# Performance work log

Measured on AMD Instinct MI355X. Metric: run time of the kernel, lower is better.

The kernel has to match this reference:

```python
import jax, jax.numpy as jnp
import numpy as np

B, G, IN, F, O = 65536, 6, 512, 256, 18


def setup_inputs() -> dict:
    key = jax.random.key(0)
    ks = jax.random.split(key, 9)
    return {
        "state": jax.random.normal(ks[0], (B, IN), dtype=jnp.float32),
        "action": jax.random.randint(ks[1], (B, 1), 0, O, dtype=jnp.int64),
        "idx": jax.random.randint(ks[2], (B,), 0, G, dtype=jnp.int64),
        # per-game expert Linear weights (stored [in, out] so fwd is x @ W)
        "W1": jax.random.normal(ks[3], (G, IN, F), dtype=jnp.float32) * (1.0 / np.sqrt(IN)),
        "b1": jnp.zeros((G, F), dtype=jnp.float32),
        # shared layer
        "W2": jax.random.normal(ks[4], (F, F), dtype=jnp.float32) * (1.0 / np.sqrt(F)),
        "b2": jnp.zeros((F,), dtype=jnp.float32),
        # per-game Q heads
        "Wq": jax.random.normal(ks[5], (G, F, O), dtype=jnp.float32) * (1.0 / np.sqrt(F)),
        "bq": jnp.zeros((G, O), dtype=jnp.float32),
    }


def reference(state, action, idx, W1, b1, W2, b2, Wq, bq):
    # The torch code processes samples grouped by np.unique(idx) and then
    # torch.cat's the groups: this is a stable sort of samples by idx value.
    perm = jnp.argsort(idx)  # jnp.argsort is stable by default
    sp = state[perm]         # [B, IN], samples in group-sorted order
    ip = idx[perm]           # [B]

    # per-game expert: compute all G tiny linears, select the routed one
    h_all = jax.nn.sigmoid(jnp.einsum('bi,gif->bgf', sp, W1) + b1)  # [B,G,F]
    h1 = jnp.take_along_axis(h_all, ip[:, None, None], axis=1)[:, 0, :]  # [B,F]

    # shared layer ('relu' branch)
    h_f = jax.nn.relu(h1 @ W2 + b2)  # [B,F]

    # stacked per-game heads
    q = jnp.tanh(jnp.einsum('bf,gfo->bgo', h_f, Wq) + bq)  # [B,G,O]

    # action gather: q_acted[b,g] = q[b,g,action[b,0]] (action in ORIGINAL order,
    # exactly as in the torch code, which gathers on the permuted-row q)
    a = jnp.broadcast_to(action[:, :1], (B, G))[..., None]  # [B,G,1]
    q_acted = jnp.take_along_axis(q, a, axis=2)[..., 0]     # [B,G]

    # idx gather (again with idx in ORIGINAL order, matching the torch code)
    q_out = jnp.take_along_axis(q_acted, idx[:, None], axis=1)[:, 0]  # [B]
    return q_out
```

## Files before the change

kernel.cpp:

```cpp
#include <hip/hip_runtime.h>
#include <math.h>

#define B_N 65536
#define G_N 6
#define IN_N 512
#define F_N 256
#define O_N 18

#define NB 256
#define CHUNK 256

#define TBM 64
#define MAXT 1030

typedef __bf16 bf16x8 __attribute__((ext_vector_type(8)));
typedef float f32x4 __attribute__((ext_vector_type(4)));

#define WS_BC     0
#define WS_BOFF   8192
#define WS_NTILES 16448
#define WS_DESC   16512
#define WS_W1F    65536
#define WS_W2F    (WS_W1F + 1572864)
#define WS_WQT    (WS_W2F + 131072)
#define WS_PERM   4194304

__device__ __forceinline__ unsigned short f2bf(float f) {
    union { float f; unsigned u; } a; a.f = f;
    unsigned r = a.u + 0x7fffu + ((a.u >> 16) & 1u);
    return (unsigned short)(r >> 16);
}
__device__ __forceinline__ unsigned pack2(float a, float b) {
    return (unsigned)f2bf(a) | ((unsigned)f2bf(b) << 16);
}
__device__ __forceinline__ bf16x8 asbf(uint4 u) {
    union { uint4 u; bf16x8 b; } c; c.u = u; return c.b;
}

__global__ void k_hist(const int* __restrict__ idx, int* __restrict__ bc) {
    __shared__ int cnt[G_N];
    int t = threadIdx.x;
    if (t < G_N) cnt[t] = 0;
    __syncthreads();
    int e = blockIdx.x * CHUNK + t;
    atomicAdd(&cnt[idx[e]], 1);
    __syncthreads();
    if (t < G_N) bc[blockIdx.x * G_N + t] = cnt[t];
}

__global__ void k_prefix(const int* __restrict__ bc, int* __restrict__ boff,
                         int* __restrict__ ntiles, int* __restrict__ desc) {
    __shared__ int sbc[NB * G_N];
    __shared__ int tot[G_N], st[G_N];
    __shared__ int tstart[G_N + 1];
    int t = threadIdx.x;
    for (int i = t; i < NB * G_N; i += 256) sbc[i] = bc[i];
    __syncthreads();
    int w = t >> 6, l = t & 63;
    for (int g = w; g < G_N; g += 4) {
        int v[4]; int s = 0;
#pragma unroll
        for (int j = 0; j < 4; j++) { v[j] = sbc[(l * 4 + j) * G_N + g]; s += v[j]; }
        int inc = s;
#pragma unroll
        for (int o = 1; o < 64; o <<= 1) { int x = __shfl_up(inc, o, 64); if (l >= o) inc += x; }
        int run = inc - s;
        if (l == 63) tot[g] = inc;
#pragma unroll
        for (int j = 0; j < 4; j++) { sbc[(l * 4 + j) * G_N + g] = run; run += v[j]; }
    }
    __syncthreads();
    if (t == 0) {
        int acc = 0;
        for (int g = 0; g < G_N; g++) { st[g] = acc; acc += tot[g]; }
        int nt = 0;
        for (int g = 0; g < G_N; g++) { tstart[g] = nt; nt += (tot[g] + TBM - 1) / TBM; }
        tstart[G_N] = nt;
        *ntiles = nt;
    }
    __syncthreads();
    for (int i = t; i < NB * G_N; i += 256) boff[i] = sbc[i] + st[i % G_N];
    int nt = tstart[G_N];
    for (int i = t; i < MAXT; i += 256) {
        int gd = 0, r0 = 0, nr = 0;
        if (i < nt) {
            int g = 0;
            while (g < G_N - 1 && i >= tstart[g + 1]) g++;
            int k = i - tstart[g];
            r0 = st[g] + k * TBM;
            int rem = tot[g] - k * TBM;
            nr = rem < TBM ? rem : TBM;
            gd = g;
        }
        desc[i * 3 + 0] = gd; desc[i * 3 + 1] = r0; desc[i * 3 + 2] = nr;
    }
}

__global__ void k_scatter(const int* __restrict__ idx, const int* __restrict__ boff,
                          int* __restrict__ perm) {
    __shared__ int wcnt[4][G_N];
    __shared__ int base[G_N];
    int t = threadIdx.x, w = t >> 6, l = t & 63;
    int e = blockIdx.x * CHUNK + t;
    int g = idx[e];
    int rank = 0;
    for (int gg = 0; gg < G_N; gg++) {
        unsigned long long m = __ballot(g == gg);
        if (g == gg) rank = __popcll(m & ((1ull << l) - 1ull));
        if (l == 0) wcnt[w][gg] = __popcll(m);
    }
    if (t < G_N) base[t] = boff[blockIdx.x * G_N + t];
    __syncthreads();
    int off = base[g] + rank;
    for (int ww = 0; ww < w; ww++) off += wcnt[ww][g];
    perm[off] = e;
}

__global__ void k_pack(const float* __restrict__ src, unsigned short* __restrict__ dst,
                       long srcZ, long dstZ) {
    int kf = blockIdx.x, w = blockIdx.y, g = blockIdx.z;
    int kfTot = gridDim.x;
    int f = threadIdx.x >> 6, l = threadIdx.x & 63;
    int lrow = l & 15, q = l >> 4;
    int n = w * 32 + f * 16 + lrow;
    int k0 = kf * 32 + q * 8;
    const float* s = src + (long)g * srcZ + (long)k0 * F_N + n;
    unsigned o[4];
#pragma unroll
    for (int j = 0; j < 4; j++)
        o[j] = pack2(s[(2 * j) * F_N], s[(2 * j + 1) * F_N]);
    unsigned short* d = dst + (long)g * dstZ +
        ((((long)w * kfTot + kf) * 2 + f) * 64 + l) * 8;
    uint4 v = { o[0], o[1], o[2], o[3] };
    *(uint4*)d = v;
}

__global__ void k_wqt(const float* __restrict__ wq, float* __restrict__ wqt) {
    int g = blockIdx.x, f = threadIdx.x;
#pragma unroll
    for (int o = 0; o < O_N; o++)
        wqt[((long)g * O_N + o) * F_N + f] = wq[((long)g * F_N + f) * O_N + o];
}

__global__ __launch_bounds__(512, 4) void k_fused(
    const float* __restrict__ state, const char* __restrict__ w1f,
    const char* __restrict__ w2f, const float* __restrict__ wqt,
    const float* __restrict__ b1, const float* __restrict__ b2,
    const float* __restrict__ bqv,
    const int* __restrict__ action, const int* __restrict__ idx,
    const int* __restrict__ perm, const int* __restrict__ desc,
    float* __restrict__ out) {
    int td = blockIdx.x;
    int g = desc[td * 3 + 0], row0 = desc[td * 3 + 1], nr = desc[td * 3 + 2];
    if (nr == 0) return;

    __shared__ __align__(16) unsigned short smA[TBM * 512];
    __shared__ float partial[TBM][9];
    __shared__ int gq[TBM], actv[TBM];
    unsigned short* smH = smA;

    int t = threadIdx.x, w = t >> 6, l = t & 63;
    int lrow = l & 15, q = l >> 4;
    int x0 = lrow & 7;

    const char* B1 = w1f + (((long)g * 8 + w) << 15) + l * 16;
    uint4 nb0 = *(const uint4*)(B1);
    uint4 nb1 = *(const uint4*)(B1 + 1024);

    if (t < TBM) {
        int pos = row0 + t; if (pos > B_N - 1) pos = B_N - 1;
        gq[t] = idx[pos];
        actv[t] = action[pos];
    }

    {
        int m = t >> 3, s = t & 7;
        int pr = row0 + m; if (pr > B_N - 1) pr = B_N - 1;
        const float* src = state + (long)perm[pr] * IN_N + s * 4;
        int cb = s >> 1, h = s & 1, mx = m & 7;
        char* rowbase = (char*)smA + m * 1024 + h * 8;
#pragma unroll
        for (int j = 0; j < 16; j++) {
            float4 v = *(const float4*)(src + j * 32);
            uint2 p = { pack2(v.x, v.y), pack2(v.z, v.w) };
            int c = (cb + j * 4) ^ mx;
            *(uint2*)(rowbase + c * 16) = p;
        }
    }
    __syncthreads();

    const char* ar[4];
#pragma unroll
    for (int i = 0; i < 4; i++) ar[i] = (const char*)smA + (i * 16 + lrow) * 1024;

    f32x4 acc[4][2];
#pragma unroll
    for (int i = 0; i < 4; i++)
#pragma unroll
        for (int j = 0; j < 2; j++) acc[i][j] = (f32x4){0.f, 0.f, 0.f, 0.f};

#pragma unroll
    for (int kf = 0; kf < 16; kf++) {
        uint4 cb0 = nb0, cb1 = nb1;
        if (kf < 15) {
            nb0 = *(const uint4*)(B1 + (kf + 1) * 2048);
            nb1 = *(const uint4*)(B1 + (kf + 1) * 2048 + 1024);
        }
        int c = ((kf * 4 + q) ^ x0) * 16;
        bf16x8 af[4];
#pragma unroll
        for (int i = 0; i < 4; i++) af[i] = *(const bf16x8*)(ar[i] + c);
        bf16x8 b0 = asbf(cb0), b1v = asbf(cb1);
#pragma unroll
        for (int i = 0; i < 4; i++) {
            acc[i][0] = __builtin_amdgcn_mfma_f32_16x16x32_bf16(af[i], b0, acc[i][0], 0, 0, 0);
            acc[i][1] = __builtin_amdgcn_mfma_f32_16x16x32_bf16(af[i], b1v, acc[i][1], 0, 0, 0);
        }
    }
    __syncthreads();

    {
        int col0 = w * 32 + lrow;
#pragma unroll
        for (int j = 0; j < 2; j++) {
            int col = col0 + j * 16;
            float bias = b1[g * F_N + col];
            int cc = col >> 3, cb2 = (col & 7) * 2;
#pragma unroll
            for (int i = 0; i < 4; i++)
#pragma unroll
                for (int r = 0; r < 4; r++) {
                    int row = i * 16 + q * 4 + r;
                    float v = acc[i][j][r] + bias;
                    float sg = 1.0f / (1.0f + __expf(-v));
                    int c = cc ^ (row & 7);
                    *(unsigned short*)((char*)smH + row * 512 + c * 16 + cb2) = f2bf(sg);
                }
        }
    }
    __syncthreads();

    const char* B2 = w2f + ((long)w << 14) + l * 16;
    const char* hr[4];
#pragma unroll
    for (int i = 0; i < 4; i++) hr[i] = (const char*)smH + (i * 16 + lrow) * 512;

    f32x4 acc2[4][2];
#pragma unroll
    for (int i = 0; i < 4; i++)
#pragma unroll
        for (int j = 0; j < 2; j++) acc2[i][j] = (f32x4){0.f, 0.f, 0.f, 0.f};

    uint4 m0 = *(const uint4*)(B2);
    uint4 m1 = *(const uint4*)(B2 + 1024);
#pragma unroll
    for (int kf = 0; kf < 8; kf++) {
        uint4 c0 = m0, c1 = m1;
        if (kf < 7) {
            m0 = *(const uint4*)(B2 + (kf + 1) * 2048);
            m1 = *(const uint4*)(B2 + (kf + 1) * 2048 + 1024);
        }
        int c = ((kf * 4 + q) ^ x0) * 16;
        bf16x8 af[4];
#pragma unroll
        for (int i = 0; i < 4; i++) af[i] = *(const bf16x8*)(hr[i] + c);
        bf16x8 b0 = asbf(c0), b1v = asbf(c1);
#pragma unroll
        for (int i = 0; i < 4; i++) {
            acc2[i][0] = __builtin_amdgcn_mfma_f32_16x16x32_bf16(af[i], b0, acc2[i][0], 0, 0, 0);
            acc2[i][1] = __builtin_amdgcn_mfma_f32_16x16x32_bf16(af[i], b1v, acc2[i][1], 0, 0, 0);
        }
    }

    {
        int col0 = w * 32 + lrow;
        float bias0 = b2[col0], bias1 = b2[col0 + 16];
#pragma unroll
        for (int i = 0; i < 4; i++)
#pragma unroll
            for (int r = 0; r < 4; r++) {
                int row = i * 16 + q * 4 + r;
                const float* wp = wqt + ((long)gq[row] * O_N + actv[row]) * F_N;
                float v0 = fmaxf(acc2[i][0][r] + bias0, 0.0f);
                float v1 = fmaxf(acc2[i][1][r] + bias1, 0.0f);
                float s = v0 * wp[col0] + v1 * wp[col0 + 16];
                s += __shfl_xor(s, 1, 64);
                s += __shfl_xor(s, 2, 64);
                s += __shfl_xor(s, 4, 64);
                s += __shfl_xor(s, 8, 64);
                if (lrow == 0) partial[row][w] = s;
            }
    }
    __syncthreads();
    if (t < TBM && t < nr) {
        float s = 0.f;
#pragma unroll
        for (int ww = 0; ww < 8; ww++) s += partial[t][ww];
        out[row0 + t] = tanhf(s + bqv[gq[t] * O_N + actv[t]]);
    }
}

extern "C" void kernel_launch(void* const* d_in, const int* in_sizes, int n_in,
                              void* d_out, int out_size, void* d_ws, size_t ws_size,
                              hipStream_t stream) {
    const float* state  = (const float*)d_in[0];
    const int*   action = (const int*)d_in[1];
    const int*   idx    = (const int*)d_in[2];
    const float* W1     = (const float*)d_in[3];
    const float* b1     = (const float*)d_in[4];
    const float* W2     = (const float*)d_in[5];
    const float* b2     = (const float*)d_in[6];
    const float* Wq     = (const float*)d_in[7];
    const float* bq     = (const float*)d_in[8];
    float* out = (float*)d_out;

    char* ws = (char*)d_ws;
    int* bc      = (int*)(ws + WS_BC);
    int* boff    = (int*)(ws + WS_BOFF);
    int* ntiles  = (int*)(ws + WS_NTILES);
    int* desc    = (int*)(ws + WS_DESC);
    unsigned short* W1f = (unsigned short*)(ws + WS_W1F);
    unsigned short* W2f = (unsigned short*)(ws + WS_W2F);
    float* WqT   = (float*)(ws + WS_WQT);
    int* perm    = (int*)(ws + WS_PERM);

    k_hist<<<NB, CHUNK, 0, stream>>>(idx, bc);
    k_prefix<<<1, 256, 0, stream>>>(bc, boff, ntiles, desc);
    k_scatter<<<NB, CHUNK, 0, stream>>>(idx, boff, perm);
    k_pack<<<dim3(IN_N / 32, 8, G_N), 128, 0, stream>>>(W1, W1f,
                                                        (long)IN_N * F_N, (long)IN_N * F_N);
    k_pack<<<dim3(F_N / 32, 8, 1), 128, 0, stream>>>(W2, W2f, 0, 0);
    k_wqt<<<G_N, 256, 0, stream>>>(Wq, WqT);
    k_fused<<<MAXT, 512, 0, stream>>>(state, (const char*)W1f, (const char*)W2f, WqT,
                                      b1, b2, bq, action, idx, perm, desc, out);
}
```

Measured before the change: 266.5 us.

## Halve fused-kernel row tile to 32 and merge weight packing into one launch

The fused MLP kernel now processes 32 rows per block instead of 64. The grid doubles, the launch-bounds occupancy hint rises from 4 to 6, and the state loading and MFMA loops are resized to match. This aims to give more blocks and better latency hiding, at the cost of half as much reuse of the expert weights per block, so more weight traffic through L2. The three weight-preparation launches (W1 pack, W2 pack, Wq transpose) are folded into a single kernel to save launch overhead.

```diff
diff --git a/kernel.cpp b/kernel.cpp
--- a/kernel.cpp
+++ b/kernel.cpp
@@ -10,8 +10,8 @@
 #define NB 256
 #define CHUNK 256
 
-#define TBM 64
-#define MAXT 1030
+#define TBM 32
+#define MAXT (B_N / TBM + G_N)
 
 typedef __bf16 bf16x8 __attribute__((ext_vector_type(8)));
 typedef float f32x4 __attribute__((ext_vector_type(4)));
@@ -116,33 +116,41 @@
     perm[off] = e;
 }
 
-__global__ void k_pack(const float* __restrict__ src, unsigned short* __restrict__ dst,
-                       long srcZ, long dstZ) {
-    int kf = blockIdx.x, w = blockIdx.y, g = blockIdx.z;
-    int kfTot = gridDim.x;
+__global__ void k_pack_all(const float* __restrict__ W1, const float* __restrict__ W2,
+                           const float* __restrict__ Wq,
+                           unsigned short* __restrict__ W1f, unsigned short* __restrict__ W2f,
+                           float* __restrict__ WqT) {
+    int kf = blockIdx.x, w = blockIdx.y, z = blockIdx.z;
+    if (z == 6 && kf >= 8) {
+        int tid = ((kf - 8) * 8 + w) * 128 + threadIdx.x;
+        for (int e = tid; e < G_N * O_N * F_N; e += 8192) {
+            int f = e & (F_N - 1);
+            int go = e >> 8;
+            int g = go / O_N, o = go - g * O_N;
+            WqT[e] = Wq[((long)g * F_N + f) * O_N + o];
+        }
+        return;
+    }
+    const float* src;
+    unsigned short* dst;
+    int kfTot;
+    if (z < 6) { src = W1 + (long)z * IN_N * F_N; dst = W1f + (long)z * IN_N * F_N; kfTot = 16; }
+    else       { src = W2; dst = W2f; kfTot = 8; }
     int f = threadIdx.x >> 6, l = threadIdx.x & 63;
     int lrow = l & 15, q = l >> 4;
     int n = w * 32 + f * 16 + lrow;
     int k0 = kf * 32 + q * 8;
-    const float* s = src + (long)g * srcZ + (long)k0 * F_N + n;
+    const float* s = src + (long)k0 * F_N + n;
     unsigned o[4];
 #pragma unroll
     for (int j = 0; j < 4; j++)
         o[j] = pack2(s[(2 * j) * F_N], s[(2 * j + 1) * F_N]);
-    unsigned short* d = dst + (long)g * dstZ +
-        ((((long)w * kfTot + kf) * 2 + f) * 64 + l) * 8;
+    unsigned short* d = dst + ((((long)w * kfTot + kf) * 2 + f) * 64 + l) * 8;
     uint4 v = { o[0], o[1], o[2], o[3] };
     *(uint4*)d = v;
 }
 
-__global__ void k_wqt(const float* __restrict__ wq, float* __restrict__ wqt) {
-    int g = blockIdx.x, f = threadIdx.x;
-#pragma unroll
-    for (int o = 0; o < O_N; o++)
-        wqt[((long)g * O_N + o) * F_N + f] = wq[((long)g * F_N + f) * O_N + o];
-}
-
-__global__ __launch_bounds__(512, 4) void k_fused(
+__global__ __launch_bounds__(512, 6) void k_fused(
     const float* __restrict__ state, const char* __restrict__ w1f,
     const char* __restrict__ w2f, const float* __restrict__ wqt,
     const float* __restrict__ b1, const float* __restrict__ b2,
@@ -174,28 +182,28 @@
     }
 
     {
-        int m = t >> 3, s = t & 7;
+        int m = t >> 4, s = t & 15;
         int pr = row0 + m; if (pr > B_N - 1) pr = B_N - 1;
         const float* src = state + (long)perm[pr] * IN_N + s * 4;
         int cb = s >> 1, h = s & 1, mx = m & 7;
         char* rowbase = (char*)smA + m * 1024 + h * 8;
 #pragma unroll
-        for (int j = 0; j < 16; j++) {
-            float4 v = *(const float4*)(src + j * 32);
+        for (int j = 0; j < 8; j++) {
+            float4 v = *(const float4*)(src + j * 64);
             uint2 p = { pack2(v.x, v.y), pack2(v.z, v.w) };
-            int c = (cb + j * 4) ^ mx;
+            int c = (cb + j * 8) ^ mx;
             *(uint2*)(rowbase + c * 16) = p;
         }
     }
     __syncthreads();
 
-    const char* ar[4];
-#pragma unroll
-    for (int i = 0; i < 4; i++) ar[i] = (const char*)smA + (i * 16 + lrow) * 1024;
-
-    f32x4 acc[4][2];
-#pragma unroll
-    for (int i = 0; i < 4; i++)
+    const char* ar[2];
+#pragma unroll
+    for (int i = 0; i < 2; i++) ar[i] = (const char*)smA + (i * 16 + lrow) * 1024;
+
+    f32x4 acc[2][2];
+#pragma unroll
+    for (int i = 0; i < 2; i++)
 #pragma unroll
         for (int j = 0; j < 2; j++) acc[i][j] = (f32x4){0.f, 0.f, 0.f, 0.f};
 
@@ -207,12 +215,12 @@
             nb1 = *(const uint4*)(B1 + (kf + 1) * 2048 + 1024);
         }
         int c = ((kf * 4 + q) ^ x0) * 16;
-        bf16x8 af[4];
-#pragma unroll
-        for (int i = 0; i < 4; i++) af[i] = *(const bf16x8*)(ar[i] + c);
+        bf16x8 af[2];
+#pragma unroll
+        for (int i = 0; i < 2; i++) af[i] = *(const bf16x8*)(ar[i] + c);
         bf16x8 b0 = asbf(cb0), b1v = asbf(cb1);
 #pragma unroll
-        for (int i = 0; i < 4; i++) {
+        for (int i = 0; i < 2; i++) {
             acc[i][0] = __builtin_amdgcn_mfma_f32_16x16x32_bf16(af[i], b0, acc[i][0], 0, 0, 0);
             acc[i][1] = __builtin_amdgcn_mfma_f32_16x16x32_bf16(af[i], b1v, acc[i][1], 0, 0, 0);
         }
@@ -227,7 +235,7 @@
             float bias = b1[g * F_N + col];
             int cc = col >> 3, cb2 = (col & 7) * 2;
 #pragma unroll
-            for (int i = 0; i < 4; i++)
+            for (int i = 0; i < 2; i++)
 #pragma unroll
                 for (int r = 0; r < 4; r++) {
                     int row = i * 16 + q * 4 + r;
@@ -241,13 +249,13 @@
     __syncthreads();
 
     const char* B2 = w2f + ((long)w << 14) + l * 16;
-    const char* hr[4];
-#pragma unroll
-    for (int i = 0; i < 4; i++) hr[i] = (const char*)smH + (i * 16 + lrow) * 512;
-
-    f32x4 acc2[4][2];
-#pragma unroll
-    for (int i = 0; i < 4; i++)
+    const char* hr[2];
+#pragma unroll
+    for (int i = 0; i < 2; i++) hr[i] = (const char*)smH + (i * 16 + lrow) * 512;
+
+    f32x4 acc2[2][2];
+#pragma unroll
+    for (int i = 0; i < 2; i++)
 #pragma unroll
         for (int j = 0; j < 2; j++) acc2[i][j] = (f32x4){0.f, 0.f, 0.f, 0.f};
 
@@ -261,12 +269,12 @@
             m1 = *(const uint4*)(B2 + (kf + 1) * 2048 + 1024);
         }
         int c = ((kf * 4 + q) ^ x0) * 16;
-        bf16x8 af[4];
-#pragma unroll
-        for (int i = 0; i < 4; i++) af[i] = *(const bf16x8*)(hr[i] + c);
+        bf16x8 af[2];
+#pragma unroll
+        for (int i = 0; i < 2; i++) af[i] = *(const bf16x8*)(hr[i] + c);
         bf16x8 b0 = asbf(c0), b1v = asbf(c1);
 #pragma unroll
-        for (int i = 0; i < 4; i++) {
+        for (int i = 0; i < 2; i++) {
             acc2[i][0] = __builtin_amdgcn_mfma_f32_16x16x32_bf16(af[i], b0, acc2[i][0], 0, 0, 0);
             acc2[i][1] = __builtin_amdgcn_mfma_f32_16x16x32_bf16(af[i], b1v, acc2[i][1], 0, 0, 0);
         }
@@ -276,7 +284,7 @@
         int col0 = w * 32 + lrow;
         float bias0 = b2[col0], bias1 = b2[col0 + 16];
 #pragma unroll
-        for (int i = 0; i < 4; i++)
+        for (int i = 0; i < 2; i++)
 #pragma unroll
             for (int r = 0; r < 4; r++) {
                 int row = i * 16 + q * 4 + r;
@@ -327,10 +335,7 @@
     k_hist<<<NB, CHUNK, 0, stream>>>(idx, bc);
     k_prefix<<<1, 256, 0, stream>>>(bc, boff, ntiles, desc);
     k_scatter<<<NB, CHUNK, 0, stream>>>(idx, boff, perm);
-    k_pack<<<dim3(IN_N / 32, 8, G_N), 128, 0, stream>>>(W1, W1f,
-                                                        (long)IN_N * F_N, (long)IN_N * F_N);
-    k_pack<<<dim3(F_N / 32, 8, 1), 128, 0, stream>>>(W2, W2f, 0, 0);
-    k_wqt<<<G_N, 256, 0, stream>>>(Wq, WqT);
+    k_pack_all<<<dim3(16, 8, 7), 128, 0, stream>>>(W1, W2, Wq, W1f, W2f, WqT);
     k_fused<<<MAXT, 512, 0, stream>>>(state, (const char*)W1f, (const char*)W2f, WqT,
                                       b1, b2, bq, action, idx, perm, desc, out);
 }
```

After: 252.2 us. 5.3% less time.
